# Optimization experiments

Hardware: AMD Instinct MI355X
Metric: run time of the kernel (lower is better)

Reference implementation:

```python
import jax, jax.numpy as jnp
import numpy as np

N_NODES = 50000
N_EDGES = 600000
IN_CH = 128
HID_CH = 128
OUT_CH = 64
NUM_GRAPHS = 512


def _gcn_conv(x, W, b, src, dst, n):
    # PyG GCNConv (eval): h = D^{-1/2} (A + I) D^{-1/2} (x W) + b
    h = x @ W  # [N, C]
    loop = jnp.arange(n)
    s = jnp.concatenate([src, loop])  # add self-loops
    d = jnp.concatenate([dst, loop])
    deg = jax.ops.segment_sum(jnp.ones_like(d, dtype=h.dtype), d, num_segments=n)
    dinv = jnp.where(deg > 0, jax.lax.rsqrt(deg), 0.0)
    coef = dinv[s] * dinv[d]  # [E+N]
    msg = h[s] * coef[:, None]  # gather + scale
    out = jax.ops.segment_sum(msg, d, num_segments=n)  # scatter-add
    return out + b


def setup_inputs() -> dict:
    key = jax.random.key(0)
    ks = jax.random.split(key, 10)
    x = jax.random.normal(ks[0], (N_NODES, IN_CH), dtype=jnp.float32)
    edge_index = jax.random.randint(ks[1], (2, N_EDGES), 0, N_NODES, dtype=jnp.int64)
    batch = jnp.sort(jax.random.randint(ks[2], (N_NODES,), 0, NUM_GRAPHS, dtype=jnp.int64))
    sc1 = 1.0 / np.sqrt(IN_CH)
    sc2 = 1.0 / np.sqrt(HID_CH)
    W1 = jax.random.uniform(ks[3], (IN_CH, HID_CH), jnp.float32, -sc1, sc1)
    b1 = jnp.zeros((HID_CH,), jnp.float32)
    W2 = jax.random.uniform(ks[4], (HID_CH, HID_CH), jnp.float32, -sc2, sc2)
    b2 = jnp.zeros((HID_CH,), jnp.float32)
    Wlin = jax.random.uniform(ks[5], (HID_CH, OUT_CH), jnp.float32, -sc2, sc2)
    blin = jax.random.uniform(ks[6], (OUT_CH,), jnp.float32, -sc2, sc2)
    return {"x": x, "W1": W1, "b1": b1, "W2": W2, "b2": b2,
            "Wlin": Wlin, "blin": blin, "edge_index": edge_index, "batch": batch}


def reference(x, W1, b1, W2, b2, Wlin, blin, edge_index, batch):
    n = x.shape[0]
    src, dst = edge_index[0], edge_index[1]
    h = jax.nn.relu(_gcn_conv(x, W1, b1, src, dst, n))
    # dropout: identity in eval mode (training=False)
    h = jax.nn.relu(_gcn_conv(h, W2, b2, src, dst, n))
    # global mean pool over graphs
    summed = jax.ops.segment_sum(h, batch, num_segments=NUM_GRAPHS)
    cnt = jax.ops.segment_sum(jnp.ones((n,), h.dtype), batch, num_segments=NUM_GRAPHS)
    pooled = summed / jnp.maximum(cnt, 1.0)[:, None]
    return pooled @ Wlin + blin  # [NUM_GRAPHS, OUT_CH]
```

## Files before the change

kernel.cpp:

```cpp
#include <hip/hip_runtime.h>

#define N_NODES 50000
#define N_EDGES 600000
#define CH 128
#define NUM_GRAPHS 512
#define OUT_CH 64
#define DSH 6
#define DSTRIDE 64

typedef unsigned int uint32;
typedef __attribute__((ext_vector_type(8))) short short8;
typedef __attribute__((ext_vector_type(4))) float floatx4;

__device__ __forceinline__ uint32 bfpack(float a, float b) {
    uint32 ua = __builtin_bit_cast(uint32, a);
    uint32 ub = __builtin_bit_cast(uint32, b);
    ua = (ua + 0x7fffu + ((ua >> 16) & 1u)) >> 16;
    ub = (ub + 0x7fffu + ((ub >> 16) & 1u)) >> 16;
    return (ub << 16) | ua;
}
__device__ __forceinline__ unsigned short bfr(float f) {
    uint32 u = __builtin_bit_cast(uint32, f);
    u = (u + 0x7fffu + ((u >> 16) & 1u)) >> 16;
    return (unsigned short)u;
}
__device__ __forceinline__ float bf_lo(uint32 v) {
    return __builtin_bit_cast(float, v << 16);
}
__device__ __forceinline__ float bf_hi(uint32 v) {
    return __builtin_bit_cast(float, v & 0xffff0000u);
}

__global__ void k_prep(const float* __restrict__ W1, const float* __restrict__ W2,
                       unsigned short* __restrict__ W1t, unsigned short* __restrict__ W2t,
                       int* __restrict__ cur) {
    int idx = blockIdx.x * 256 + threadIdx.x;
    if (idx < N_NODES) cur[idx] = 0;
    if (idx < 32768) {
        int mat = idx >> 14;
        int rem = idx & 16383;
        int k = rem >> 7, c = rem & 127;
        const float* W = mat ? W2 : W1;
        unsigned short* Wt = mat ? W2t : W1t;
        Wt[c * 128 + k] = bfr(W[k * 128 + c]);
    }
}

__global__ void k_fill_pad(const int4* __restrict__ src4, const int4* __restrict__ dst4,
                           int* __restrict__ cur, int* __restrict__ srcs) {
    int e4 = blockIdx.x * 256 + threadIdx.x;
    if (e4 < N_EDGES / 4) {
        int4 s = src4[e4];
        int4 d = dst4[e4];
        int p;
        p = atomicAdd(&cur[d.x], 1); srcs[(d.x << DSH) + p] = s.x;
        p = atomicAdd(&cur[d.y], 1); srcs[(d.y << DSH) + p] = s.y;
        p = atomicAdd(&cur[d.z], 1); srcs[(d.z << DSH) + p] = s.z;
        p = atomicAdd(&cur[d.w], 1); srcs[(d.w << DSH) + p] = s.w;
    }
}

template <bool AF32>
__global__ __launch_bounds__(256, 2) void k_gemm(const void* __restrict__ Av,
                                                 const unsigned short* __restrict__ Wt,
                                                 const int* __restrict__ cur,
                                                 unsigned short* __restrict__ outb) {
    __shared__ __align__(16) unsigned short as_[128][136];
    __shared__ __align__(16) unsigned short bs[128][136];
    int tid = threadIdx.x;
    int row0 = blockIdx.x * 128;

    #pragma unroll
    for (int it = 0; it < 8; ++it) {
        int idx = it * 256 + tid;
        int r = idx >> 4, seg = idx & 15;
        int gr = min(row0 + r, N_NODES - 1);
        if (AF32) {
            const float4* ap = (const float4*)((const float*)Av + (size_t)gr * 128 + seg * 8);
            float4 v0 = ap[0], v1 = ap[1];
            uint4 pk;
            pk.x = bfpack(v0.x, v0.y); pk.y = bfpack(v0.z, v0.w);
            pk.z = bfpack(v1.x, v1.y); pk.w = bfpack(v1.z, v1.w);
            *(uint4*)&as_[r][seg * 8] = pk;
        } else {
            *(uint4*)&as_[r][seg * 8] =
                *(const uint4*)((const unsigned short*)Av + (size_t)gr * 128 + seg * 8);
        }
    }
    #pragma unroll
    for (int it = 0; it < 8; ++it) {
        int idx = it * 256 + tid;
        int c = idx >> 4, seg = idx & 15;
        *(uint4*)&bs[c][seg * 8] = *(const uint4*)&Wt[c * 128 + seg * 8];
    }
    __syncthreads();

    int w = tid >> 6, lane = tid & 63, q = lane >> 4, m = lane & 15;
    int q8 = q * 8;
    floatx4 acc[2][8];
    #pragma unroll
    for (int rt = 0; rt < 2; ++rt)
        #pragma unroll
        for (int ct = 0; ct < 8; ++ct) {
            floatx4 z = {0.f, 0.f, 0.f, 0.f};
            acc[rt][ct] = z;
        }

    #pragma unroll
    for (int kc = 0; kc < 128; kc += 32) {
        short8 a0 = *(const short8*)&as_[w * 32 + m][kc + q8];
        short8 a1 = *(const short8*)&as_[w * 32 + 16 + m][kc + q8];
        #pragma unroll
        for (int ct = 0; ct < 8; ++ct) {
            short8 b = *(const short8*)&bs[ct * 16 + m][kc + q8];
            acc[0][ct] = __builtin_amdgcn_mfma_f32_16x16x32_bf16(a0, b, acc[0][ct], 0, 0, 0);
            acc[1][ct] = __builtin_amdgcn_mfma_f32_16x16x32_bf16(a1, b, acc[1][ct], 0, 0, 0);
        }
    }

    #pragma unroll
    for (int rt = 0; rt < 2; ++rt) {
        #pragma unroll
        for (int i = 0; i < 4; ++i) {
            int gr = row0 + w * 32 + rt * 16 + q * 4 + i;
            if (gr < N_NODES) {
                float sc = rsqrtf((float)(cur[gr] + 1));
                #pragma unroll
                for (int ct = 0; ct < 8; ++ct) {
                    outb[(size_t)gr * 128 + ct * 16 + m] = bfr(acc[rt][ct][i] * sc);
                }
            }
        }
    }
}

template <bool BF16OUT>
__global__ __launch_bounds__(256) void k_agg(const uint32* __restrict__ hb,
                                             const int* __restrict__ cnt_arr,
                                             const int* __restrict__ srcs,
                                             const float* __restrict__ bias,
                                             void* __restrict__ outv) {
    int node = __builtin_amdgcn_readfirstlane(blockIdx.x * 4 + (threadIdx.x >> 6));
    int lane = threadIdx.x & 63;

    int cnt = cnt_arr[node];
    float dn = rsqrtf((float)(cnt + 1));
    uint32 vs = hb[node * 64 + lane];
    float ax = bf_lo(vs), ay = bf_hi(vs);

    int start = node << DSH;
    int last = start + cnt - 1;
    for (int j = 0; j < cnt; j += 8) {
        int i0 = start + j;
        int i1 = min(i0 + 1, last);
        int i2 = min(i0 + 2, last);
        int i3 = min(i0 + 3, last);
        int i4 = min(i0 + 4, last);
        int i5 = min(i0 + 5, last);
        int i6 = min(i0 + 6, last);
        int i7 = min(i0 + 7, last);
        int s0 = srcs[i0], s1 = srcs[i1], s2 = srcs[i2], s3 = srcs[i3];
        int s4 = srcs[i4], s5 = srcs[i5], s6 = srcs[i6], s7 = srcs[i7];
        uint32 v0 = hb[s0 * 64 + lane];
        uint32 v1 = hb[s1 * 64 + lane];
        uint32 v2 = hb[s2 * 64 + lane];
        uint32 v3 = hb[s3 * 64 + lane];
        uint32 v4 = hb[s4 * 64 + lane];
        uint32 v5 = hb[s5 * 64 + lane];
        uint32 v6 = hb[s6 * 64 + lane];
        uint32 v7 = hb[s7 * 64 + lane];
        int rem = cnt - j;
        v1 = (rem > 1) ? v1 : 0u;
        v2 = (rem > 2) ? v2 : 0u;
        v3 = (rem > 3) ? v3 : 0u;
        v4 = (rem > 4) ? v4 : 0u;
        v5 = (rem > 5) ? v5 : 0u;
        v6 = (rem > 6) ? v6 : 0u;
        v7 = (rem > 7) ? v7 : 0u;
        ax += bf_lo(v0); ay += bf_hi(v0);
        ax += bf_lo(v1); ay += bf_hi(v1);
        ax += bf_lo(v2); ay += bf_hi(v2);
        ax += bf_lo(v3); ay += bf_hi(v3);
        ax += bf_lo(v4); ay += bf_hi(v4);
        ax += bf_lo(v5); ay += bf_hi(v5);
        ax += bf_lo(v6); ay += bf_hi(v6);
        ax += bf_lo(v7); ay += bf_hi(v7);
    }
    float2 b = ((const float2*)bias)[lane];
    ax = fmaxf(ax * dn + b.x, 0.f);
    ay = fmaxf(ay * dn + b.y, 0.f);
    if (BF16OUT) ((uint32*)outv)[node * 64 + lane] = bfpack(ax, ay);
    else         ((float2*)outv)[node * 64 + lane] = make_float2(ax, ay);
}

__global__ __launch_bounds__(256) void k_pool_linear(const float* __restrict__ h,
                                                     const int* __restrict__ batch,
                                                     const float* __restrict__ Wl,
                                                     const float* __restrict__ bl,
                                                     float* __restrict__ out) {
    __shared__ int sb[2];
    __shared__ float4 sacc[256];
    __shared__ float xr[CH];
    __shared__ float po[4][OUT_CH];
    int g = blockIdx.x;
    int tid = threadIdx.x;
    if (tid < 2) {
        int target = g + tid;
        int lo = 0, hi = N_NODES;
        while (lo < hi) {
            int mid = (lo + hi) >> 1;
            if (batch[mid] < target) lo = mid + 1; else hi = mid;
        }
        sb[tid] = lo;
    }
    __syncthreads();
    int lo = sb[0], hi = sb[1];
    int q = tid & 31;
    int r = tid >> 5;
    const float4* h4 = (const float4*)h;
    float4 acc = make_float4(0.f, 0.f, 0.f, 0.f);
    for (int i = lo + r; i < hi; i += 8) {
        float4 v = h4[(size_t)i * 32 + q];
        acc.x += v.x; acc.y += v.y; acc.z += v.z; acc.w += v.w;
    }
    sacc[tid] = acc;
    __syncthreads();
    if (r == 0) {
        #pragma unroll
        for (int p = 1; p < 8; ++p) {
            float4 t = sacc[q + p * 32];
            acc.x += t.x; acc.y += t.y; acc.z += t.z; acc.w += t.w;
        }
        float inv = 1.f / (float)((hi - lo) > 0 ? (hi - lo) : 1);
        xr[q * 4 + 0] = acc.x * inv;
        xr[q * 4 + 1] = acc.y * inv;
        xr[q * 4 + 2] = acc.z * inv;
        xr[q * 4 + 3] = acc.w * inv;
    }
    __syncthreads();
    int c = tid & 63;
    int kh = tid >> 6;
    float o = 0.f;
    #pragma unroll 8
    for (int k = kh * 32; k < kh * 32 + 32; ++k) o += xr[k] * Wl[k * OUT_CH + c];
    po[kh][c] = o;
    __syncthreads();
    if (tid < OUT_CH) {
        float v = bl[tid] + po[0][tid] + po[1][tid] + po[2][tid] + po[3][tid];
        out[g * OUT_CH + tid] = v;
    }
}

extern "C" void kernel_launch(void* const* d_in, const int* in_sizes, int n_in,
                              void* d_out, int out_size, void* d_ws, size_t ws_size,
                              hipStream_t stream) {
    const float* x    = (const float*)d_in[0];
    const float* W1   = (const float*)d_in[1];
    const float* b1   = (const float*)d_in[2];
    const float* W2   = (const float*)d_in[3];
    const float* b2   = (const float*)d_in[4];
    const float* Wlin = (const float*)d_in[5];
    const float* blin = (const float*)d_in[6];
    const int* ei     = (const int*)d_in[7];
    const int* batch  = (const int*)d_in[8];
    const int* esrc = ei;
    const int* edst = ei + N_EDGES;
    float* out = (float*)d_out;

    char* w = (char*)d_ws;
    size_t o = 0;
    float* hA            = (float*)(w + o);          o += (size_t)N_NODES * CH * 4;
    unsigned short* hb   = (unsigned short*)(w + o); o += (size_t)N_NODES * CH * 2;
    uint32* habf         = (uint32*)(w + o);         o += (size_t)N_NODES * 64 * 4;
    unsigned short* W1t  = (unsigned short*)(w + o); o += 16384 * 2;
    unsigned short* W2t  = (unsigned short*)(w + o); o += 16384 * 2;
    int* srcs            = (int*)(w + o);            o += (size_t)N_NODES * DSTRIDE * 4;
    int* cur             = (int*)(w + o);            o += 200704;
    (void)ws_size; (void)in_sizes; (void)n_in; (void)out_size;

    dim3 b256(256);
    k_prep<<<dim3(196), b256, 0, stream>>>(W1, W2, W1t, W2t, cur);
    k_fill_pad<<<dim3((N_EDGES / 4 + 255) / 256), b256, 0, stream>>>(
        (const int4*)esrc, (const int4*)edst, cur, srcs);

    dim3 gG((N_NODES + 127) / 128);
    dim3 gA(N_NODES / 4);
    k_gemm<true><<<gG, b256, 0, stream>>>(x, W1t, cur, hb);
    k_agg<true><<<gA, b256, 0, stream>>>((const uint32*)hb, cur, srcs, b1, habf);
    k_gemm<false><<<gG, b256, 0, stream>>>(habf, W2t, cur, hb);
    k_agg<false><<<gA, b256, 0, stream>>>((const uint32*)hb, cur, srcs, b2, hA);
    k_pool_linear<<<dim3(NUM_GRAPHS), b256, 0, stream>>>(hA, batch, Wlin, blin, out);
}
```

Baseline: 200.8 us.

## Fuse edge bucketing into first GEMM and move source-degree scaling into aggregation

Measured after the change: 211.6 us. 5.4% more time.

```diff
diff --git a/kernel.cpp b/kernel.cpp
--- a/kernel.cpp
+++ b/kernel.cpp
@@ -7,6 +7,8 @@
 #define OUT_CH 64
 #define DSH 6
 #define DSTRIDE 64
+#define FILL_BLOCKS ((N_EDGES / 4 + 255) / 256)
+#define GEMM_BLOCKS ((N_NODES + 127) / 128)
 
 typedef unsigned int uint32;
 typedef __attribute__((ext_vector_type(8))) short short8;
@@ -46,29 +48,33 @@
     }
 }
 
-__global__ void k_fill_pad(const int4* __restrict__ src4, const int4* __restrict__ dst4,
-                           int* __restrict__ cur, int* __restrict__ srcs) {
-    int e4 = blockIdx.x * 256 + threadIdx.x;
-    if (e4 < N_EDGES / 4) {
-        int4 s = src4[e4];
-        int4 d = dst4[e4];
-        int p;
-        p = atomicAdd(&cur[d.x], 1); srcs[(d.x << DSH) + p] = s.x;
-        p = atomicAdd(&cur[d.y], 1); srcs[(d.y << DSH) + p] = s.y;
-        p = atomicAdd(&cur[d.z], 1); srcs[(d.z << DSH) + p] = s.z;
-        p = atomicAdd(&cur[d.w], 1); srcs[(d.w << DSH) + p] = s.w;
-    }
-}
-
-template <bool AF32>
+template <bool AF32, bool FUSED_FILL>
 __global__ __launch_bounds__(256, 2) void k_gemm(const void* __restrict__ Av,
                                                  const unsigned short* __restrict__ Wt,
-                                                 const int* __restrict__ cur,
-                                                 unsigned short* __restrict__ outb) {
+                                                 unsigned short* __restrict__ outb,
+                                                 const int4* __restrict__ src4,
+                                                 const int4* __restrict__ dst4,
+                                                 int* __restrict__ cur,
+                                                 int* __restrict__ srcs) {
+    if (FUSED_FILL) {
+        if (blockIdx.x < FILL_BLOCKS) {
+            int e4 = blockIdx.x * 256 + threadIdx.x;
+            if (e4 < N_EDGES / 4) {
+                int4 s = src4[e4];
+                int4 d = dst4[e4];
+                int p;
+                p = atomicAdd(&cur[d.x], 1); srcs[(d.x << DSH) + p] = s.x;
+                p = atomicAdd(&cur[d.y], 1); srcs[(d.y << DSH) + p] = s.y;
+                p = atomicAdd(&cur[d.z], 1); srcs[(d.z << DSH) + p] = s.z;
+                p = atomicAdd(&cur[d.w], 1); srcs[(d.w << DSH) + p] = s.w;
+            }
+            return;
+        }
+    }
     __shared__ __align__(16) unsigned short as_[128][136];
     __shared__ __align__(16) unsigned short bs[128][136];
     int tid = threadIdx.x;
-    int row0 = blockIdx.x * 128;
+    int row0 = (blockIdx.x - (FUSED_FILL ? FILL_BLOCKS : 0)) * 128;
 
     #pragma unroll
     for (int it = 0; it < 8; ++it) {
@@ -124,10 +130,9 @@
         for (int i = 0; i < 4; ++i) {
             int gr = row0 + w * 32 + rt * 16 + q * 4 + i;
             if (gr < N_NODES) {
-                float sc = rsqrtf((float)(cur[gr] + 1));
                 #pragma unroll
                 for (int ct = 0; ct < 8; ++ct) {
-                    outb[(size_t)gr * 128 + ct * 16 + m] = bfr(acc[rt][ct][i] * sc);
+                    outb[(size_t)gr * 128 + ct * 16 + m] = bfr(acc[rt][ct][i]);
                 }
             }
         }
@@ -146,7 +151,7 @@
     int cnt = cnt_arr[node];
     float dn = rsqrtf((float)(cnt + 1));
     uint32 vs = hb[node * 64 + lane];
-    float ax = bf_lo(vs), ay = bf_hi(vs);
+    float ax = bf_lo(vs) * dn, ay = bf_hi(vs) * dn;
 
     int start = node << DSH;
     int last = start + cnt - 1;
@@ -161,6 +166,8 @@
         int i7 = min(i0 + 7, last);
         int s0 = srcs[i0], s1 = srcs[i1], s2 = srcs[i2], s3 = srcs[i3];
         int s4 = srcs[i4], s5 = srcs[i5], s6 = srcs[i6], s7 = srcs[i7];
+        int c0 = cnt_arr[s0], c1 = cnt_arr[s1], c2 = cnt_arr[s2], c3 = cnt_arr[s3];
+        int c4 = cnt_arr[s4], c5 = cnt_arr[s5], c6 = cnt_arr[s6], c7 = cnt_arr[s7];
         uint32 v0 = hb[s0 * 64 + lane];
         uint32 v1 = hb[s1 * 64 + lane];
         uint32 v2 = hb[s2 * 64 + lane];
@@ -169,6 +176,14 @@
         uint32 v5 = hb[s5 * 64 + lane];
         uint32 v6 = hb[s6 * 64 + lane];
         uint32 v7 = hb[s7 * 64 + lane];
+        float d0 = rsqrtf((float)(c0 + 1));
+        float d1 = rsqrtf((float)(c1 + 1));
+        float d2 = rsqrtf((float)(c2 + 1));
+        float d3 = rsqrtf((float)(c3 + 1));
+        float d4 = rsqrtf((float)(c4 + 1));
+        float d5 = rsqrtf((float)(c5 + 1));
+        float d6 = rsqrtf((float)(c6 + 1));
+        float d7 = rsqrtf((float)(c7 + 1));
         int rem = cnt - j;
         v1 = (rem > 1) ? v1 : 0u;
         v2 = (rem > 2) ? v2 : 0u;
@@ -177,14 +192,14 @@
         v5 = (rem > 5) ? v5 : 0u;
         v6 = (rem > 6) ? v6 : 0u;
         v7 = (rem > 7) ? v7 : 0u;
-        ax += bf_lo(v0); ay += bf_hi(v0);
-        ax += bf_lo(v1); ay += bf_hi(v1);
-        ax += bf_lo(v2); ay += bf_hi(v2);
-        ax += bf_lo(v3); ay += bf_hi(v3);
-        ax += bf_lo(v4); ay += bf_hi(v4);
-        ax += bf_lo(v5); ay += bf_hi(v5);
-        ax += bf_lo(v6); ay += bf_hi(v6);
-        ax += bf_lo(v7); ay += bf_hi(v7);
+        ax = fmaf(d0, bf_lo(v0), ax); ay = fmaf(d0, bf_hi(v0), ay);
+        ax = fmaf(d1, bf_lo(v1), ax); ay = fmaf(d1, bf_hi(v1), ay);
+        ax = fmaf(d2, bf_lo(v2), ax); ay = fmaf(d2, bf_hi(v2), ay);
+        ax = fmaf(d3, bf_lo(v3), ax); ay = fmaf(d3, bf_hi(v3), ay);
+        ax = fmaf(d4, bf_lo(v4), ax); ay = fmaf(d4, bf_hi(v4), ay);
+        ax = fmaf(d5, bf_lo(v5), ax); ay = fmaf(d5, bf_hi(v5), ay);
+        ax = fmaf(d6, bf_lo(v6), ax); ay = fmaf(d6, bf_hi(v6), ay);
+        ax = fmaf(d7, bf_lo(v7), ax); ay = fmaf(d7, bf_hi(v7), ay);
     }
     float2 b = ((const float2*)bias)[lane];
     ax = fmaxf(ax * dn + b.x, 0.f);
@@ -280,14 +295,15 @@
 
     dim3 b256(256);
     k_prep<<<dim3(196), b256, 0, stream>>>(W1, W2, W1t, W2t, cur);
-    k_fill_pad<<<dim3((N_EDGES / 4 + 255) / 256), b256, 0, stream>>>(
+
+    dim3 gGF(FILL_BLOCKS + GEMM_BLOCKS);
+    dim3 gG(GEMM_BLOCKS);
+    dim3 gA(N_NODES / 4);
+    k_gemm<true, true><<<gGF, b256, 0, stream>>>(x, W1t, hb,
         (const int4*)esrc, (const int4*)edst, cur, srcs);
-
-    dim3 gG((N_NODES + 127) / 128);
-    dim3 gA(N_NODES / 4);
-    k_gemm<true><<<gG, b256, 0, stream>>>(x, W1t, cur, hb);
     k_agg<true><<<gA, b256, 0, stream>>>((const uint32*)hb, cur, srcs, b1, habf);
-    k_gemm<false><<<gG, b256, 0, stream>>>(habf, W2t, cur, hb);
+    k_gemm<false, false><<<gG, b256, 0, stream>>>(habf, W2t, hb,
+        nullptr, nullptr, cur, srcs);
     k_agg<false><<<gA, b256, 0, stream>>>((const uint32*)hb, cur, srcs, b2, hA);
     k_pool_linear<<<dim3(NUM_GRAPHS), b256, 0, stream>>>(hA, batch, Wlin, blin, out);
 }
```

## Partition edge fill by destination slice to localize atomics and scatter writes

Applied to the files above, without the earlier changes.

Result: no change. 197.0 us (-1.9%).

```diff
diff --git a/kernel.cpp b/kernel.cpp
--- a/kernel.cpp
+++ b/kernel.cpp
@@ -7,6 +7,10 @@
 #define OUT_CH 64
 #define DSH 6
 #define DSTRIDE 64
+#define PF_GROUPS 8
+#define PF_BPG 75
+#define PF_E4_PER_BLOCK (N_EDGES / 4 / PF_BPG)
+#define PF_SLICE (N_NODES / PF_GROUPS)
 
 typedef unsigned int uint32;
 typedef __attribute__((ext_vector_type(8))) short short8;
@@ -46,17 +50,23 @@
     }
 }
 
-__global__ void k_fill_pad(const int4* __restrict__ src4, const int4* __restrict__ dst4,
-                           int* __restrict__ cur, int* __restrict__ srcs) {
-    int e4 = blockIdx.x * 256 + threadIdx.x;
-    if (e4 < N_EDGES / 4) {
+__global__ __launch_bounds__(256) void k_fill_part(const int4* __restrict__ src4,
+                                                   const int4* __restrict__ dst4,
+                                                   int* __restrict__ cur,
+                                                   int* __restrict__ srcs) {
+    int g = blockIdx.x & (PF_GROUPS - 1);
+    int cb = blockIdx.x >> 3;
+    int lo = g * PF_SLICE;
+    int hi = lo + PF_SLICE;
+    int base = cb * PF_E4_PER_BLOCK;
+    for (int i = threadIdx.x; i < PF_E4_PER_BLOCK; i += 256) {
+        int e4 = base + i;
+        int4 d = dst4[e4];
         int4 s = src4[e4];
-        int4 d = dst4[e4];
-        int p;
-        p = atomicAdd(&cur[d.x], 1); srcs[(d.x << DSH) + p] = s.x;
-        p = atomicAdd(&cur[d.y], 1); srcs[(d.y << DSH) + p] = s.y;
-        p = atomicAdd(&cur[d.z], 1); srcs[(d.z << DSH) + p] = s.z;
-        p = atomicAdd(&cur[d.w], 1); srcs[(d.w << DSH) + p] = s.w;
+        if (d.x >= lo && d.x < hi) { int p = atomicAdd(&cur[d.x], 1); srcs[(d.x << DSH) + p] = s.x; }
+        if (d.y >= lo && d.y < hi) { int p = atomicAdd(&cur[d.y], 1); srcs[(d.y << DSH) + p] = s.y; }
+        if (d.z >= lo && d.z < hi) { int p = atomicAdd(&cur[d.z], 1); srcs[(d.z << DSH) + p] = s.z; }
+        if (d.w >= lo && d.w < hi) { int p = atomicAdd(&cur[d.w], 1); srcs[(d.w << DSH) + p] = s.w; }
     }
 }
 
@@ -280,7 +290,7 @@
 
     dim3 b256(256);
     k_prep<<<dim3(196), b256, 0, stream>>>(W1, W2, W1t, W2t, cur);
-    k_fill_pad<<<dim3((N_EDGES / 4 + 255) / 256), b256, 0, stream>>>(
+    k_fill_part<<<dim3(PF_GROUPS * PF_BPG), b256, 0, stream>>>(
         (const int4*)esrc, (const int4*)edst, cur, srcs);
 
     dim3 gG((N_NODES + 127) / 128);
```
